# Kernel tuning notes

Hardware: AMD Instinct MI355X
Metric: run time of the kernel (lower is better)

Reference implementation:

```python
import jax, jax.numpy as jnp
import numpy as np

MARGIN = 1.0


def setup_inputs() -> dict:
    key = jax.random.key(0)
    k1, k2, k3 = jax.random.split(key, 3)
    B, D = 4096, 256
    N = 2 * B
    out_a = jax.random.normal(k1, (B, D), dtype=jnp.float32)
    out_b = jax.random.normal(k2, (B, D), dtype=jnp.float32)
    # one random negative index per row, uniform over the N-2 masked (valid) columns
    neg_choice = jax.random.randint(k3, (N,), 0, N - 2, dtype=jnp.int32)
    return {"out_a": out_a, "out_b": out_b, "neg_choice": neg_choice}


def reference(out_a, out_b, neg_choice):
    B = out_a.shape[0]
    N = 2 * B
    features = jnp.concatenate([out_a, out_b], axis=0)  # [N, D]

    # berg_div
    idx_max = jnp.argmax(features, axis=1)                       # [N]
    max_feat = jnp.max(features, axis=1, keepdims=True)          # [N, 1]
    num_max = jnp.zeros((features.shape[1],), dtype=features.dtype).at[idx_max].add(1.0)
    dist = max_feat - features[:, idx_max]                       # [N, N]

    # positives: diagonals at offsets +B / -B
    pos_ab = jnp.diagonal(dist, offset=B)    # [B]
    pos_ba = jnp.diagonal(dist, offset=-B)   # [B]
    positives = jnp.concatenate([pos_ab, pos_ba], axis=0)        # [N]

    # one random negative per row: masked columns of row i exclude {i, pair(i)}.
    # Map neg_choice j in [0, N-2) to actual column by skipping the two excluded cols.
    rows = jnp.arange(N)
    pair = (rows + B) % N
    e1 = jnp.minimum(rows, pair)
    e2 = jnp.maximum(rows, pair)
    c = neg_choice
    c = c + (c >= e1).astype(c.dtype)
    c = c + (c >= e2).astype(c.dtype)
    negatives = dist[rows, c]                                    # [N]

    # criterion: pos + clamp(margin - neg, 0)^2, summed, /2
    mdist = jnp.maximum(MARGIN - negatives, 0.0)
    loss = jnp.sum(positives + mdist * mdist) / 2.0
    return (loss, num_max)
```

## Files before the change

### kernel.cpp

```cpp
#include <hip/hip_runtime.h>

#define BB 4096
#define NN 8192
#define DD 256

__global__ void rowmax_kernel(const float* __restrict__ out_a,
                              const float* __restrict__ out_b,
                              float* __restrict__ max_feat,
                              int* __restrict__ idx_max,
                              float* __restrict__ num_max ) {
    int gtid = blockIdx.x * blockDim.x + threadIdx.x;
    int row  = gtid >> 6;
    int lane = threadIdx.x & 63;
    if (row >= NN) return;

    const float* rowp = (row < BB) ? (out_a + (size_t)row * DD)
                                   : (out_b + (size_t)(row - BB) * DD);
    float4 v = *reinterpret_cast<const float4*>(rowp + lane * 4);

    float best = v.x; int bi = lane * 4;
    if (v.y > best) { best = v.y; bi = lane * 4 + 1; }
    if (v.z > best) { best = v.z; bi = lane * 4 + 2; }
    if (v.w > best) { best = v.w; bi = lane * 4 + 3; }

    #pragma unroll
    for (int off = 32; off >= 1; off >>= 1) {
        float ov = __shfl_xor(best, off, 64);
        int   oi = __shfl_xor(bi,   off, 64);
        if (ov > best || (ov == best && oi < bi)) { best = ov; bi = oi; }
    }

    if (lane == 0) {
        max_feat[row] = best;
        idx_max[row]  = bi;
        atomicAdd(&num_max[bi], 1.0f);
    }
}

__global__ void loss_kernel(const float* __restrict__ out_a,
                            const float* __restrict__ out_b,
                            const int* __restrict__ neg_choice,
                            const float* __restrict__ max_feat,
                            const int* __restrict__ idx_max,
                            float* __restrict__ loss ) {
    int r = blockIdx.x * blockDim.x + threadIdx.x;
    float term = 0.0f;
    if (r < NN) {
        int pair = (r < BB) ? (r + BB) : (r - BB);
        int e1   = (r < BB) ? r : (r - BB);
        int e2   = e1 + BB;
        int c = neg_choice[r];
        c += (c >= e1);
        c += (c >= e2);

        const float* rowp = (r < BB) ? (out_a + (size_t)r * DD)
                                     : (out_b + (size_t)(r - BB) * DD);
        float mf  = max_feat[r];
        float pos = mf - rowp[idx_max[pair]];
        float neg = mf - rowp[idx_max[c]];
        float md  = fmaxf(1.0f - neg, 0.0f);
        term = pos + md * md;
    }
    #pragma unroll
    for (int off = 32; off >= 1; off >>= 1)
        term += __shfl_xor(term, off, 64);
    if ((threadIdx.x & 63) == 0)
        atomicAdd(loss, 0.5f * term);
}

extern "C" void kernel_launch(void* const* d_in, const int* in_sizes, int n_in,
                              void* d_out, int out_size, void* d_ws, size_t ws_size,
                              hipStream_t stream) {
    const float* out_a      = (const float*)d_in[0];
    const float* out_b      = (const float*)d_in[1];
    const int*   neg_choice = (const int*)d_in[2];
    float* out = (float*)d_out;

    float* max_feat = (float*)d_ws;
    int*   idx_max  = (int*)((char*)d_ws + NN * sizeof(float));

    hipMemsetAsync(d_out, 0, (size_t)out_size * sizeof(float), stream);

    rowmax_kernel<<<NN / 4, 256, 0, stream>>>(out_a, out_b, max_feat, idx_max, out + 1);

    loss_kernel<<<NN / 256, 256, 0, stream>>>(out_a, out_b, neg_choice,
                                              max_feat, idx_max, out);
}
```

Before: 82.62 us.

## Replace memset and global atomics with single-block finish kernel

```diff
diff --git a/kernel.cpp b/kernel.cpp
--- a/kernel.cpp
+++ b/kernel.cpp
@@ -7,8 +7,7 @@
 __global__ void rowmax_kernel(const float* __restrict__ out_a,
                               const float* __restrict__ out_b,
                               float* __restrict__ max_feat,
-                              int* __restrict__ idx_max,
-                              float* __restrict__ num_max ) {
+                              int* __restrict__ idx_max) {
     int gtid = blockIdx.x * blockDim.x + threadIdx.x;
     int row  = gtid >> 6;
     int lane = threadIdx.x & 63;
@@ -33,39 +32,56 @@
     if (lane == 0) {
         max_feat[row] = best;
         idx_max[row]  = bi;
-        atomicAdd(&num_max[bi], 1.0f);
     }
 }
 
-__global__ void loss_kernel(const float* __restrict__ out_a,
-                            const float* __restrict__ out_b,
-                            const int* __restrict__ neg_choice,
-                            const float* __restrict__ max_feat,
-                            const int* __restrict__ idx_max,
-                            float* __restrict__ loss ) {
-    int r = blockIdx.x * blockDim.x + threadIdx.x;
-    float term = 0.0f;
-    if (r < NN) {
-        int pair = (r < BB) ? (r + BB) : (r - BB);
-        int e1   = (r < BB) ? r : (r - BB);
+__global__ void __launch_bounds__(256)
+finish_kernel(const float* __restrict__ out_a,
+              const float* __restrict__ out_b,
+              const int* __restrict__ neg_choice,
+              const float* __restrict__ max_feat,
+              const int* __restrict__ idx_max,
+              float* __restrict__ out ) {
+    __shared__ int   s_idx[NN];
+    __shared__ int   s_hist[DD];
+    __shared__ float s_part[4];
+
+    int tid = threadIdx.x;
+
+    for (int i = tid; i < NN; i += 256) s_idx[i] = idx_max[i];
+    s_hist[tid] = 0;
+    __syncthreads();
+
+    for (int i = tid; i < NN; i += 256) atomicAdd(&s_hist[s_idx[i]], 1);
+
+    float acc = 0.0f;
+    for (int i = tid; i < NN; i += 256) {
+        int pair = (i < BB) ? (i + BB) : (i - BB);
+        int e1   = (i < BB) ? i : (i - BB);
         int e2   = e1 + BB;
-        int c = neg_choice[r];
+        int c = neg_choice[i];
         c += (c >= e1);
         c += (c >= e2);
 
-        const float* rowp = (r < BB) ? (out_a + (size_t)r * DD)
-                                     : (out_b + (size_t)(r - BB) * DD);
-        float mf  = max_feat[r];
-        float pos = mf - rowp[idx_max[pair]];
-        float neg = mf - rowp[idx_max[c]];
+        const float* rowp = (i < BB) ? (out_a + (size_t)i * DD)
+                                     : (out_b + (size_t)(i - BB) * DD);
+        float mf  = max_feat[i];
+        float pos = mf - rowp[s_idx[pair]];
+        float neg = mf - rowp[s_idx[c]];
         float md  = fmaxf(1.0f - neg, 0.0f);
-        term = pos + md * md;
+        acc += pos + md * md;
     }
+
+    __syncthreads();
+    out[1 + tid] = (float)s_hist[tid];
+
     #pragma unroll
     for (int off = 32; off >= 1; off >>= 1)
-        term += __shfl_xor(term, off, 64);
-    if ((threadIdx.x & 63) == 0)
-        atomicAdd(loss, 0.5f * term);
+        acc += __shfl_xor(acc, off, 64);
+    if ((tid & 63) == 0) s_part[tid >> 6] = acc;
+    __syncthreads();
+    if (tid == 0)
+        out[0] = 0.5f * (s_part[0] + s_part[1] + s_part[2] + s_part[3]);
 }
 
 extern "C" void kernel_launch(void* const* d_in, const int* in_sizes, int n_in,
@@ -79,10 +95,8 @@
     float* max_feat = (float*)d_ws;
     int*   idx_max  = (int*)((char*)d_ws + NN * sizeof(float));
 
-    hipMemsetAsync(d_out, 0, (size_t)out_size * sizeof(float), stream);
+    rowmax_kernel<<<NN / 4, 256, 0, stream>>>(out_a, out_b, max_feat, idx_max);
 
-    rowmax_kernel<<<NN / 4, 256, 0, stream>>>(out_a, out_b, max_feat, idx_max, out + 1);
-
-    loss_kernel<<<NN / 256, 256, 0, stream>>>(out_a, out_b, neg_choice,
-                                              max_feat, idx_max, out);
+    finish_kernel<<<1, 256, 0, stream>>>(out_a, out_b, neg_choice,
+                                         max_feat, idx_max, out);
 }
```

After: 95.37 us. 15.4% more time.
